# Kernel tuning notes

Hardware: AMD Instinct MI355X
Metric: run time of the kernel (lower is better)

Reference implementation:

```python
import jax, jax.numpy as jnp
import numpy as np

BETA = 0.25
NUM_EMB = 50
EMB_DIM = 192


def setup_inputs() -> dict:
    key = jax.random.key(0)
    k1, k2 = jax.random.split(key)
    N = 262144
    inputs = jax.random.normal(k1, (N, EMB_DIM), dtype=jnp.float32)
    # nn.Embedding init: uniform(-1/num_embeddings, 1/num_embeddings)
    embed_w = jax.random.uniform(k2, (NUM_EMB, EMB_DIM), dtype=jnp.float32,
                                 minval=-1.0 / NUM_EMB, maxval=1.0 / NUM_EMB)
    return {"inputs": inputs, "embed_w": embed_w}


def reference(inputs, embed_w):
    # flat_input: [N, D] (inputs already flattened to last-dim = embedding_dim)
    flat = inputs.reshape(-1, EMB_DIM)
    distances = (jnp.sum(flat * flat, axis=1, keepdims=True)
                 + jnp.sum(embed_w * embed_w, axis=1)
                 - 2.0 * (flat @ embed_w.T))
    encoding_indices = jnp.argmin(distances, axis=1)[:, None]  # [N, 1]
    # one-hot scatter + matmul in the original == direct gather of nearest code
    quantized = embed_w[encoding_indices[:, 0]]  # [N, D]
    sg = jax.lax.stop_gradient
    commitloss = (jnp.mean((sg(quantized) - flat) ** 2)
                  + BETA * jnp.mean((quantized - sg(flat)) ** 2))
    # straight-through estimator
    quantized_st = flat + sg(quantized - flat)
    contrastloss = jnp.float32(0.0)
    return (quantized_st, encoding_indices, commitloss, contrastloss)
```

## Files before the change

### kernel.cpp

```cpp
#include <hip/hip_runtime.h>
#include <cfloat>

#define NUM_EMB 50
#define EMB_DIM 192
#define ESTRIDE 196

__device__ __forceinline__ float np_tree8(const float r[8]) {
#pragma clang fp contract(off)
    return ((r[0] + r[1]) + (r[2] + r[3])) + ((r[4] + r[5]) + (r[6] + r[7]));
}

__device__ float np_sumsq_192(const float* __restrict__ p) {
#pragma clang fp contract(off)
    float tot[2];
#pragma unroll
    for (int h = 0; h < 2; ++h) {
        float r[8];
#pragma unroll
        for (int l = 0; l < 8; ++l) r[l] = 0.f;
        const float* q = p + h * 96;
        for (int t = 0; t < 12; ++t)
#pragma unroll
            for (int l = 0; l < 8; ++l) {
                float v = q[t * 8 + l];
                float pr = v * v;
                r[l] = r[l] + pr;
            }
        tot[h] = np_tree8(r);
    }
    return tot[0] + tot[1];
}

__global__ __launch_bounds__(256, 4) void vq_main(
    const float* __restrict__ x, const float* __restrict__ ew,
    float* __restrict__ out_idx, float* __restrict__ out_loss, int N)
{
    __shared__ float sE[NUM_EMB * EMB_DIM];
    __shared__ float sB[NUM_EMB];

    for (int i = threadIdx.x; i < NUM_EMB * EMB_DIM; i += blockDim.x)
        sE[i] = ew[i];
    __syncthreads();
    if (threadIdx.x < NUM_EMB)
        sB[threadIdx.x] = np_sumsq_192(&sE[threadIdx.x * EMB_DIM]);
    __syncthreads();

    const int row = blockIdx.x * blockDim.x + threadIdx.x;
    const float4* xr = (const float4*)(x + (size_t)row * EMB_DIM);

    float acc[NUM_EMB];
#pragma unroll
    for (int k = 0; k < NUM_EMB; ++k) acc[k] = 0.f;

    float rA[8];
    float aHalf[2];

    for (int m = 0; m < 6; ++m) {
        float4 f4[8];
#pragma unroll
        for (int q = 0; q < 8; ++q) f4[q] = xr[m * 8 + q];

        if ((m % 3) == 0) {
#pragma unroll
            for (int l = 0; l < 8; ++l) rA[l] = 0.f;
        }
        {
#pragma clang fp contract(off)
#pragma unroll
            for (int q = 0; q < 8; ++q) {
                float p0 = f4[q].x * f4[q].x; rA[(q * 4 + 0) & 7] = rA[(q * 4 + 0) & 7] + p0;
                float p1 = f4[q].y * f4[q].y; rA[(q * 4 + 1) & 7] = rA[(q * 4 + 1) & 7] + p1;
                float p2 = f4[q].z * f4[q].z; rA[(q * 4 + 2) & 7] = rA[(q * 4 + 2) & 7] + p2;
                float p3 = f4[q].w * f4[q].w; rA[(q * 4 + 3) & 7] = rA[(q * 4 + 3) & 7] + p3;
            }
        }
        if ((m % 3) == 2) aHalf[m / 3] = np_tree8(rA);

        const float* eb = &sE[m * 32];
#pragma unroll
        for (int k = 0; k < NUM_EMB; ++k) {
            const float* ek = eb + k * EMB_DIM;
#pragma unroll
            for (int q = 0; q < 8; ++q) {
                const float4 e4 = *(const float4*)&ek[q * 4];
                acc[k] = __builtin_fmaf(f4[q].x, e4.x, acc[k]);
                acc[k] = __builtin_fmaf(f4[q].y, e4.y, acc[k]);
                acc[k] = __builtin_fmaf(f4[q].z, e4.z, acc[k]);
                acc[k] = __builtin_fmaf(f4[q].w, e4.w, acc[k]);
            }
        }
    }

    float best; int bidx;
    {
#pragma clang fp contract(off)
        float a = aHalf[0] + aHalf[1];
        best = FLT_MAX; bidx = 0;
#pragma unroll
        for (int k = 0; k < NUM_EMB; ++k) {
            float t1 = a + sB[k];
            float u  = 2.0f * acc[k];
            float d  = t1 - u;
            if (d < best) { best = d; bidx = k; }
        }
    }
    out_idx[row] = (float)bidx;

    float contrib = best;
#pragma unroll
    for (int off = 1; off < 64; off <<= 1) contrib += __shfl_xor(contrib, off);
    if ((threadIdx.x & 63) == 0) atomicAdd(out_loss, contrib);
}

__global__ __launch_bounds__(256, 4) void vq_gather(
    const float* __restrict__ ew, const float* __restrict__ out_idx,
    float* __restrict__ out_q, int N)
{
    __shared__ __align__(16) float sE[NUM_EMB * ESTRIDE];
    for (int i = threadIdx.x; i < NUM_EMB * EMB_DIM; i += blockDim.x) {
        int k = i / EMB_DIM, j = i - k * EMB_DIM;
        sE[k * ESTRIDE + j] = ew[i];
    }
    __syncthreads();

    const int lane = threadIdx.x & 63;
    const int wave = threadIdx.x >> 6;
    const int c = lane & 7;
    const int r = lane >> 3;
    const int waves_total = gridDim.x * (blockDim.x >> 6);
    const int wave_gid = blockIdx.x * (blockDim.x >> 6) + wave;
    const int ngroups = N >> 3;

    for (int g = wave_gid; g < ngroups; g += waves_total) {
        const int row = g * 8 + r;
        const int bidx = (int)out_idx[row];
        float4* qrow = (float4*)(out_q + (size_t)row * EMB_DIM);
        const float* erow = &sE[bidx * ESTRIDE];
#pragma unroll
        for (int t = 0; t < 6; ++t)
            qrow[c + 8 * t] = *(const float4*)&erow[(c + 8 * t) * 4];
    }
}

__global__ void vq_init(float* out_loss) { out_loss[0] = 0.f; out_loss[1] = 0.f; }

__global__ void vq_finalize(float* __restrict__ out_loss, int N)
{
    double mean = (double)out_loss[0] / ((double)N * (double)EMB_DIM);
    out_loss[0] = (float)(1.25 * mean);
    out_loss[1] = 0.f;
}

extern "C" void kernel_launch(void* const* d_in, const int* in_sizes, int n_in,
                              void* d_out, int out_size, void* d_ws, size_t ws_size,
                              hipStream_t stream)
{
    const float* x  = (const float*)d_in[0];
    const float* ew = (const float*)d_in[1];
    const int N = in_sizes[0] / EMB_DIM;

    float* out_q    = (float*)d_out;
    float* out_idx  = out_q + (size_t)N * EMB_DIM;
    float* out_loss = out_idx + N;

    vq_init<<<1, 1, 0, stream>>>(out_loss);
    vq_main<<<N / 256, 256, 0, stream>>>(x, ew, out_idx, out_loss, N);
    vq_gather<<<2048, 256, 0, stream>>>(ew, out_idx, out_q, N);
    vq_finalize<<<1, 1, 0, stream>>>(out_loss, N);
}
```

Before: 439.0 us.

## Fuse gather into main kernel and read codebook from global memory

Merges the separate gather kernel into the distance kernel. Each wave broadcasts its argmin indices with shuffles and writes the quantized rows from a padded shared-memory codebook. The dot-product loop now reads codebook vectors from global memory (uniform addresses, served through the scalar or L1 path) instead of LDS, with eight float4 loads batched per code. This removes a kernel launch and the re-read of indices, and frees LDS bandwidth in the inner loop. The cost is that inner-loop throughput now depends on how cache-friendly and uniform those global loads are.

```diff
diff --git a/kernel.cpp b/kernel.cpp
--- a/kernel.cpp
+++ b/kernel.cpp
@@ -31,18 +31,21 @@
     return tot[0] + tot[1];
 }
 
-__global__ __launch_bounds__(256, 4) void vq_main(
+__global__ __launch_bounds__(256, 4) void vq_fused(
     const float* __restrict__ x, const float* __restrict__ ew,
-    float* __restrict__ out_idx, float* __restrict__ out_loss, int N)
+    float* __restrict__ out_q, float* __restrict__ out_idx,
+    float* __restrict__ out_loss, int N)
 {
-    __shared__ float sE[NUM_EMB * EMB_DIM];
+    __shared__ __align__(16) float sE[NUM_EMB * ESTRIDE];
     __shared__ float sB[NUM_EMB];
 
-    for (int i = threadIdx.x; i < NUM_EMB * EMB_DIM; i += blockDim.x)
-        sE[i] = ew[i];
+    for (int i = threadIdx.x; i < NUM_EMB * EMB_DIM; i += blockDim.x) {
+        int k = i / EMB_DIM, j = i - k * EMB_DIM;
+        sE[k * ESTRIDE + j] = ew[i];
+    }
     __syncthreads();
     if (threadIdx.x < NUM_EMB)
-        sB[threadIdx.x] = np_sumsq_192(&sE[threadIdx.x * EMB_DIM]);
+        sB[threadIdx.x] = np_sumsq_192(&sE[threadIdx.x * ESTRIDE]);
     __syncthreads();
 
     const int row = blockIdx.x * blockDim.x + threadIdx.x;
@@ -76,17 +79,19 @@
         }
         if ((m % 3) == 2) aHalf[m / 3] = np_tree8(rA);
 
-        const float* eb = &sE[m * 32];
+        const float* eb = ew + m * 32;
 #pragma unroll
         for (int k = 0; k < NUM_EMB; ++k) {
             const float* ek = eb + k * EMB_DIM;
+            float4 e4[8];
+#pragma unroll
+            for (int q = 0; q < 8; ++q) e4[q] = *(const float4*)&ek[q * 4];
 #pragma unroll
             for (int q = 0; q < 8; ++q) {
-                const float4 e4 = *(const float4*)&ek[q * 4];
-                acc[k] = __builtin_fmaf(f4[q].x, e4.x, acc[k]);
-                acc[k] = __builtin_fmaf(f4[q].y, e4.y, acc[k]);
-                acc[k] = __builtin_fmaf(f4[q].z, e4.z, acc[k]);
-                acc[k] = __builtin_fmaf(f4[q].w, e4.w, acc[k]);
+                acc[k] = __builtin_fmaf(f4[q].x, e4[q].x, acc[k]);
+                acc[k] = __builtin_fmaf(f4[q].y, e4[q].y, acc[k]);
+                acc[k] = __builtin_fmaf(f4[q].z, e4[q].z, acc[k]);
+                acc[k] = __builtin_fmaf(f4[q].w, e4[q].w, acc[k]);
             }
         }
     }
@@ -110,35 +115,22 @@
 #pragma unroll
     for (int off = 1; off < 64; off <<= 1) contrib += __shfl_xor(contrib, off);
     if ((threadIdx.x & 63) == 0) atomicAdd(out_loss, contrib);
-}
 
-__global__ __launch_bounds__(256, 4) void vq_gather(
-    const float* __restrict__ ew, const float* __restrict__ out_idx,
-    float* __restrict__ out_q, int N)
-{
-    __shared__ __align__(16) float sE[NUM_EMB * ESTRIDE];
-    for (int i = threadIdx.x; i < NUM_EMB * EMB_DIM; i += blockDim.x) {
-        int k = i / EMB_DIM, j = i - k * EMB_DIM;
-        sE[k * ESTRIDE + j] = ew[i];
-    }
-    __syncthreads();
-
-    const int lane = threadIdx.x & 63;
-    const int wave = threadIdx.x >> 6;
-    const int c = lane & 7;
-    const int r = lane >> 3;
-    const int waves_total = gridDim.x * (blockDim.x >> 6);
-    const int wave_gid = blockIdx.x * (blockDim.x >> 6) + wave;
-    const int ngroups = N >> 3;
-
-    for (int g = wave_gid; g < ngroups; g += waves_total) {
-        const int row = g * 8 + r;
-        const int bidx = (int)out_idx[row];
-        float4* qrow = (float4*)(out_q + (size_t)row * EMB_DIM);
-        const float* erow = &sE[bidx * ESTRIDE];
+    {
+        const int lane = threadIdx.x & 63;
+        const int c = lane & 7;
+        const int rr = lane >> 3;
+        const int waveRow0 = row & ~63;
 #pragma unroll
-        for (int t = 0; t < 6; ++t)
-            qrow[c + 8 * t] = *(const float4*)&erow[(c + 8 * t) * 4];
+        for (int g = 0; g < 8; ++g) {
+            const int kk = __shfl(bidx, g * 8 + rr);
+            const int wrow = waveRow0 + g * 8 + rr;
+            float4* qrow = (float4*)(out_q + (size_t)wrow * EMB_DIM);
+            const float* erow = &sE[kk * ESTRIDE];
+#pragma unroll
+            for (int t = 0; t < 6; ++t)
+                qrow[c + 8 * t] = *(const float4*)&erow[(c + 8 * t) * 4];
+        }
     }
 }
 
@@ -164,7 +156,6 @@
     float* out_loss = out_idx + N;
 
     vq_init<<<1, 1, 0, stream>>>(out_loss);
-    vq_main<<<N / 256, 256, 0, stream>>>(x, ew, out_idx, out_loss, N);
-    vq_gather<<<2048, 256, 0, stream>>>(ew, out_idx, out_q, N);
+    vq_fused<<<N / 256, 256, 0, stream>>>(x, ew, out_q, out_idx, out_loss, N);
     vq_finalize<<<1, 1, 0, stream>>>(out_loss, N);
 }
```

Measured after the change: 420.1 us. 1.05x faster.
